# Kernel tuning notes

Measured on AMD Instinct MI355X. Metric: run time of the kernel, lower is better.

The kernel has to match this reference:

```python
import jax, jax.numpy as jnp
import numpy as np

B, L, E, R, A = 1024, 40, 1024, 1024, 512


def setup_inputs() -> dict:
    key = jax.random.key(0)
    ks = jax.random.split(key, 20)
    s = 0.05  # weight scale to avoid gate saturation
    inp = {
        "xt": jax.random.normal(ks[0], (B, E), jnp.float32),
        "xt_mask": jnp.ones((B, 1), jnp.float32),
        "V": jax.random.normal(ks[1], (B, L, R), jnp.float32),
        "pos_feat": jax.random.normal(ks[2], (B, R), jnp.float32),
        "h1": jax.random.normal(ks[3], (1, B, R), jnp.float32),
        "c1": jax.random.normal(ks[4], (1, B, R), jnp.float32),
        "h2": jax.random.normal(ks[5], (1, B, R), jnp.float32),
        "c2": jax.random.normal(ks[6], (1, B, R), jnp.float32),
        "Wg": jax.random.normal(ks[7], (E, R), jnp.float32) * s,
        "bg": jnp.zeros((R,), jnp.float32),
        "Wi1": jax.random.normal(ks[8], (E, 4 * R), jnp.float32) * s,
        "bi1": jnp.zeros((4 * R,), jnp.float32),
        "Wa1": jax.random.normal(ks[9], (R, 4 * R), jnp.float32) * s,
        "ba1": jnp.zeros((4 * R,), jnp.float32),
        "Wh1": jax.random.normal(ks[10], (R, 4 * R), jnp.float32) * s,
        "bh1": jnp.zeros((4 * R,), jnp.float32),
        "Wi2": jax.random.normal(ks[11], (R, 4 * R), jnp.float32) * s,
        "bi2": jnp.zeros((4 * R,), jnp.float32),
        "Wa2": jax.random.normal(ks[12], (R, 4 * R), jnp.float32) * s,
        "ba2": jnp.zeros((4 * R,), jnp.float32),
        "Wh2": jax.random.normal(ks[13], (R, 4 * R), jnp.float32) * s,
        "bh2": jnp.zeros((4 * R,), jnp.float32),
        "Wv2a": jax.random.normal(ks[14], (R, A), jnp.float32) * s,
        "bv2a": jnp.zeros((A,), jnp.float32),
        "Wh2a": jax.random.normal(ks[15], (2 * R, A), jnp.float32) * s,
        "bh2a": jnp.zeros((A,), jnp.float32),
        "Wa2w": jax.random.normal(ks[16], (A, 1), jnp.float32) * s,
        "ba2w": jnp.zeros((1,), jnp.float32),
    }
    return inp


def _lstm_cell(in1, in2, h, c, Wi, bi, Wa, ba, Wh, bh, mask):
    # all_input_sums: [B, 4R]; torch gate order: i, f, o (sigmoid) then g (tanh)
    s = in1 @ Wi + bi + in2 @ Wa + ba + h @ Wh + bh
    i_g = jax.nn.sigmoid(s[:, 0 * R:1 * R])
    f_g = jax.nn.sigmoid(s[:, 1 * R:2 * R])
    o_g = jax.nn.sigmoid(s[:, 2 * R:3 * R])
    g = jnp.tanh(s[:, 3 * R:4 * R])
    c_new = f_g * c + i_g * g
    c_new = c_new * mask + c * (1.0 - mask)
    h_new = o_g * jnp.tanh(c_new)
    h_new = h_new * mask + h * (1.0 - mask)
    return h_new, c_new


def reference(xt, xt_mask, V, pos_feat, h1, c1, h2, c2,
              Wg, bg, Wi1, bi1, Wa1, ba1, Wh1, bh1,
              Wi2, bi2, Wa2, ba2, Wh2, bh2,
              Wv2a, bv2a, Wh2a, bh2a, Wa2w, ba2w):
    h1l, c1l = h1[-1], c1[-1]  # [B, R]
    h2l, c2l = h2[-1], c2[-1]
    # additive attention over L frames
    hq = jnp.concatenate([h1l, h2l], axis=1) @ Wh2a + bh2a        # [B, A]
    e = jnp.tanh(hq[:, None, :] + V @ Wv2a + bv2a) @ Wa2w + ba2w  # [B, L, 1]
    w = jax.nn.softmax(e, axis=1)                                  # softmax over L
    af = jnp.sum(w * V, axis=1)                                    # [B, R]
    # gate (dropout in eval mode -> identity)
    gate = jax.nn.relu(xt @ Wg + bg)
    gated_pos = gate * pos_feat + pos_feat
    # two-layer LSTM
    out1, c1n = _lstm_cell(xt, gated_pos, h1l, c1l, Wi1, bi1, Wa1, ba1, Wh1, bh1, xt_mask)
    out2, c2n = _lstm_cell(out1, af, h2l, c2l, Wi2, bi2, Wa2, ba2, Wh2, bh2, xt_mask)
    return (out2, out1[None], c1n[None], out2[None], c2n[None])
```

## Files before the change

kernel.cpp:

```cpp
#include <hip/hip_runtime.h>
#include <math.h>

#define BB 1024
#define LL 40
#define RR 1024

using short8 = __attribute__((ext_vector_type(8))) short;
using us8    = __attribute__((ext_vector_type(8))) unsigned short;
using f32x4  = __attribute__((ext_vector_type(4))) float;

__device__ __forceinline__ ushort f2bf(float f) {
    union { float f; unsigned u; } a; a.f = f;
    unsigned r = a.u + 0x7fffu + ((a.u >> 16) & 1u);
    return (ushort)(r >> 16);
}
__device__ __forceinline__ float bf2f(ushort u) {
    union { unsigned u; float f; } a; a.u = ((unsigned)u) << 16;
    return a.f;
}
__device__ __forceinline__ float ftanh(float x) {
    float cx = fminf(fmaxf(x, -15.f), 15.f);
    float e = __expf(2.f * cx);
    return (e - 1.f) / (e + 1.f);
}
__device__ __forceinline__ float fsigmoid(float x) {
    float cx = fminf(fmaxf(x, -30.f), 30.f);
    return 1.f / (1.f + __expf(-cx));
}

__global__ __launch_bounds__(256) void conv_bf16_kernel(
    const float* __restrict__ src, ushort* __restrict__ dst, int n8)
{
    const int i = blockIdx.x * 256 + threadIdx.x;
    if (i >= n8) return;
    const float4* s4 = (const float4*)(src + (size_t)i * 8);
    float4 x = s4[0], y = s4[1];
    us8 v;
    v[0] = f2bf(x.x); v[1] = f2bf(x.y); v[2] = f2bf(x.z); v[3] = f2bf(x.w);
    v[4] = f2bf(y.x); v[5] = f2bf(y.y); v[6] = f2bf(y.z); v[7] = f2bf(y.w);
    ((us8*)dst)[i] = v;
}

struct CP3 { const float* in[3]; ushort* out[3]; };
__global__ __launch_bounds__(256) void conv_bf16_batch3_kernel(CP3 p, int n8)
{
    const int z = blockIdx.y;
    const int i = blockIdx.x * 256 + threadIdx.x;
    if (i >= n8) return;
    const float4* s4 = (const float4*)(p.in[z] + (size_t)i * 8);
    float4 x = s4[0], y = s4[1];
    us8 v;
    v[0] = f2bf(x.x); v[1] = f2bf(x.y); v[2] = f2bf(x.z); v[3] = f2bf(x.w);
    v[4] = f2bf(y.x); v[5] = f2bf(y.y); v[6] = f2bf(y.z); v[7] = f2bf(y.w);
    ((us8*)p.out[z])[i] = v;
}

struct TP6 { const float* in[6]; ushort* out[6]; int N[6]; };
__global__ __launch_bounds__(256) void transpose_conv_kernel(TP6 p)
{
    const int z = blockIdx.z;
    const int Nn = p.N[z];
    const int n0 = blockIdx.x * 64;
    if (n0 >= Nn) return;
    const int k0 = blockIdx.y * 64;
    const float* in = p.in[z];
    ushort* out = p.out[z];

    __shared__ float tile[64][65];
    const int t = threadIdx.x;
    const int tx = t & 63, ty = t >> 6;
#pragma unroll
    for (int r = 0; r < 16; ++r) {
        const int row = ty * 16 + r;
        tile[row][tx] = in[(size_t)(k0 + row) * Nn + n0 + tx];
    }
    __syncthreads();
    const int n = t >> 2, kq = t & 3;
    us8 v0, v1;
#pragma unroll
    for (int j = 0; j < 8; ++j) v0[j] = f2bf(tile[kq * 16 + j][n]);
#pragma unroll
    for (int j = 0; j < 8; ++j) v1[j] = f2bf(tile[kq * 16 + 8 + j][n]);
    ushort* op = out + (size_t)(n0 + n) * 1024 + k0 + kq * 16;
    *(us8*)op = v0;
    *((us8*)op + 1) = v1;
}

template <int NP, int EPI, int SK>
__global__ __launch_bounds__(256) void gemm_bf16(
    const ushort* __restrict__ A0, const ushort* __restrict__ A1, const ushort* __restrict__ A2,
    const ushort* __restrict__ W0, const ushort* __restrict__ W1, const ushort* __restrict__ W2,
    const float* __restrict__ b0, const float* __restrict__ b1, const float* __restrict__ b2,
    float* __restrict__ C, int M, int N,
    const float* __restrict__ hq, const float* __restrict__ bv2a,
    const float* __restrict__ Wa2w, float* __restrict__ epart)
{
    __shared__ ushort Alds[128 * 72];
    __shared__ ushort Blds[128 * 72];
    __shared__ float  red2[128][2];

    const int t = threadIdx.x;
    const int lane = t & 63;
    const int wave = t >> 6;
    const int wm = wave >> 1, wn = wave & 1;

    int bx, by;
    if constexpr (EPI == 2) {
        const int lin = blockIdx.y * 4 + blockIdx.x;
        const int nl = (lin & 7) * 160 + (lin >> 3);
        bx = nl & 3; by = nl >> 2;
    } else {
        bx = blockIdx.x; by = blockIdx.y;
    }
    const int m0 = by * 128, n0 = bx * 128;

    const int srow = t >> 1, skh = t & 1;
    const int soff = srow * 72 + skh * 32;

    f32x4 acc[4][4];
#pragma unroll
    for (int i = 0; i < 4; ++i)
#pragma unroll
        for (int j = 0; j < 4; ++j) acc[i][j] = (f32x4){0.f, 0.f, 0.f, 0.f};

    const int total = NP * 16;
    const int per   = total / SK;
    const int s0    = blockIdx.z * per;
    const int sEnd  = s0 + per;

    short8 ra[4], rw[4];
    {
        const int p  = (NP == 1) ? 0 : (s0 >> 4);
        const int k0 = (s0 & 15) << 6;
        const ushort* Ap = (p == 0) ? A0 : ((p == 1) ? A1 : A2);
        const ushort* Wp = (p == 0) ? W0 : ((p == 1) ? W1 : W2);
        const short8* ag = (const short8*)(Ap + (size_t)(m0 + srow) * 1024 + k0 + skh * 32);
        const short8* wg = (const short8*)(Wp + (size_t)(n0 + srow) * 1024 + k0 + skh * 32);
#pragma unroll
        for (int j = 0; j < 4; ++j) { ra[j] = ag[j]; rw[j] = wg[j]; }
    }

    for (int s = s0; s < sEnd; ++s) {
        __syncthreads();
#pragma unroll
        for (int j = 0; j < 4; ++j) {
            *(short8*)&Alds[soff + j * 8] = ra[j];
            *(short8*)&Blds[soff + j * 8] = rw[j];
        }
        __syncthreads();

        if (s + 1 < sEnd) {
            const int sn = s + 1;
            const int p  = (NP == 1) ? 0 : (sn >> 4);
            const int k0 = (sn & 15) << 6;
            const ushort* Ap = (p == 0) ? A0 : ((p == 1) ? A1 : A2);
            const ushort* Wp = (p == 0) ? W0 : ((p == 1) ? W1 : W2);
            const short8* ag = (const short8*)(Ap + (size_t)(m0 + srow) * 1024 + k0 + skh * 32);
            const short8* wg = (const short8*)(Wp + (size_t)(n0 + srow) * 1024 + k0 + skh * 32);
#pragma unroll
            for (int j = 0; j < 4; ++j) { ra[j] = ag[j]; rw[j] = wg[j]; }
        }

#pragma unroll
        for (int ks = 0; ks < 2; ++ks) {
            short8 aF[4], bF[4];
#pragma unroll
            for (int mi = 0; mi < 4; ++mi)
                aF[mi] = *(const short8*)&Alds[(wm * 64 + mi * 16 + (lane & 15)) * 72 + ks * 32 + (lane >> 4) * 8];
#pragma unroll
            for (int ni = 0; ni < 4; ++ni)
                bF[ni] = *(const short8*)&Blds[(wn * 64 + ni * 16 + (lane & 15)) * 72 + ks * 32 + (lane >> 4) * 8];
#pragma unroll
            for (int mi = 0; mi < 4; ++mi)
#pragma unroll
                for (int ni = 0; ni < 4; ++ni)
                    acc[mi][ni] = __builtin_amdgcn_mfma_f32_16x16x32_bf16(aF[mi], bF[ni], acc[mi][ni], 0, 0, 0);
        }
    }

    if constexpr (EPI == 0) {
#pragma unroll
        for (int ni = 0; ni < 4; ++ni) {
            const int col = n0 + wn * 64 + ni * 16 + (lane & 15);
            float bs = b0[col];
            if (NP > 1) bs += b1[col];
            if (NP > 2) bs += b2[col];
#pragma unroll
            for (int mi = 0; mi < 4; ++mi) {
                const int row = m0 + wm * 64 + mi * 16 + ((lane >> 4) << 2);
#pragma unroll
                for (int r = 0; r < 4; ++r)
                    C[(size_t)(row + r) * N + col] = acc[mi][ni][r] + bs;
            }
        }
    } else if constexpr (EPI == 3) {
        float* Cz = C + (size_t)blockIdx.z * M * N;
#pragma unroll
        for (int ni = 0; ni < 4; ++ni) {
            const int col = n0 + wn * 64 + ni * 16 + (lane & 15);
#pragma unroll
            for (int mi = 0; mi < 4; ++mi) {
                const int row = m0 + wm * 64 + mi * 16 + ((lane >> 4) << 2);
#pragma unroll
                for (int r = 0; r < 4; ++r)
                    Cz[(size_t)(row + r) * N + col] = acc[mi][ni][r];
            }
        }
    } else if constexpr (EPI == 2) {
        float wa[4], bv[4];
        int coln[4];
#pragma unroll
        for (int ni = 0; ni < 4; ++ni) {
            coln[ni] = n0 + wn * 64 + ni * 16 + (lane & 15);
            wa[ni] = Wa2w[coln[ni]];
            bv[ni] = bv2a[coln[ni]];
        }
#pragma unroll
        for (int mi = 0; mi < 4; ++mi) {
            const int rowb = m0 + wm * 64 + mi * 16 + ((lane >> 4) << 2);
#pragma unroll
            for (int r = 0; r < 4; ++r) {
                const int row = rowb + r;
                const int b = row / LL;
                float v = 0.f;
#pragma unroll
                for (int ni = 0; ni < 4; ++ni) {
                    float x = acc[mi][ni][r] + hq[(size_t)b * 512 + coln[ni]] + bv[ni];
                    v += ftanh(x) * wa[ni];
                }
                v += __shfl_xor(v, 1);
                v += __shfl_xor(v, 2);
                v += __shfl_xor(v, 4);
                v += __shfl_xor(v, 8);
                if ((lane & 15) == 0) red2[rowb - m0 + r][wn] = v;
            }
        }
        __syncthreads();
        if (t < 128)
            epart[(size_t)(m0 + t) * 4 + bx] = red2[t][0] + red2[t][1];
    }
}

__global__ __launch_bounds__(256) void reduce_hq_kernel(
    const float* __restrict__ part, const float* __restrict__ bias, float* __restrict__ hq)
{
    const int i = blockIdx.x * 256 + threadIdx.x;
    float s = bias[i & 511];
#pragma unroll
    for (int z = 0; z < 8; ++z) s += part[(size_t)z * 524288 + i];
    hq[i] = s;
}

__global__ __launch_bounds__(256) void reduce_gate_kernel(
    const float* __restrict__ part, const float* __restrict__ bias,
    const float* __restrict__ pos, ushort* __restrict__ gpb)
{
    const int i = blockIdx.x * 256 + threadIdx.x;
    float s = bias[i & 1023];
#pragma unroll
    for (int z = 0; z < 4; ++z) s += part[(size_t)z * 1048576 + i];
    const float g = fmaxf(s, 0.f);
    gpb[i] = f2bf(g * pos[i] + pos[i]);
}

__global__ __launch_bounds__(256) void softmax_af_kernel(
    const float* __restrict__ epart, const ushort* __restrict__ Vb,
    const float* __restrict__ ba2w, ushort* __restrict__ afb)
{
    const int b = blockIdx.x;
    const int tid = threadIdx.x;
    __shared__ float e_raw[LL];
    __shared__ float e_exp[LL];

    if (tid < LL) {
        const float* ep = &epart[(size_t)(b * LL + tid) * 4];
        float e = ba2w[0];
#pragma unroll
        for (int c = 0; c < 4; ++c) e += ep[c];
        e_raw[tid] = e;
    }
    __syncthreads();
    float mx = -1e30f;
#pragma unroll
    for (int l = 0; l < LL; ++l) mx = fmaxf(mx, e_raw[l]);
    if (tid < LL) e_exp[tid] = __expf(e_raw[tid] - mx);
    __syncthreads();
    float sum = 0.f;
#pragma unroll
    for (int l = 0; l < LL; ++l) sum += e_exp[l];
    const float inv = 1.f / sum;

    const int r4 = tid * 4;
    const ushort* vp = &Vb[(size_t)b * LL * RR + r4];
    float a0 = 0.f, a1 = 0.f, a2 = 0.f, a3 = 0.f;
#pragma unroll 8
    for (int l = 0; l < LL; ++l) {
        ushort4 v = *(const ushort4*)&vp[(size_t)l * RR];
        const float w = e_exp[l];
        a0 += w * bf2f(v.x); a1 += w * bf2f(v.y);
        a2 += w * bf2f(v.z); a3 += w * bf2f(v.w);
    }
    ushort* op = &afb[(size_t)b * RR + r4];
    op[0] = f2bf(a0 * inv); op[1] = f2bf(a1 * inv);
    op[2] = f2bf(a2 * inv); op[3] = f2bf(a3 * inv);
}

__global__ __launch_bounds__(256) void lstm_finish_kernel(
    const float* __restrict__ s, const float* __restrict__ c_in,
    const float* __restrict__ h_in, const float* __restrict__ mask,
    float* __restrict__ h_out, float* __restrict__ h_out2,
    float* __restrict__ c_out, ushort* __restrict__ h_bf)
{
    const int i = blockIdx.x * 256 + threadIdx.x;
    const int b = i >> 10;
    const int r = i & 1023;
    const float* sb = &s[(size_t)b * 4 * RR];
    const float ig = fsigmoid(sb[r]);
    const float fg = fsigmoid(sb[RR + r]);
    const float og = fsigmoid(sb[2 * RR + r]);
    const float g  = ftanh(sb[3 * RR + r]);
    const float m = mask[b];
    const float c = c_in[i];
    float cn = fg * c + ig * g;
    cn = cn * m + c * (1.f - m);
    const float h = h_in[i];
    float hn = og * ftanh(cn);
    hn = hn * m + h * (1.f - m);
    h_out[i] = hn;
    if (h_out2) h_out2[i] = hn;
    c_out[i] = cn;
    if (h_bf) h_bf[i] = f2bf(hn);
}

extern "C" void kernel_launch(void* const* d_in, const int* in_sizes, int n_in,
                              void* d_out, int out_size, void* d_ws, size_t ws_size,
                              hipStream_t stream) {
    const float* xt   = (const float*)d_in[0];
    const float* mask = (const float*)d_in[1];
    const float* V    = (const float*)d_in[2];
    const float* pos  = (const float*)d_in[3];
    const float* h1   = (const float*)d_in[4];
    const float* c1   = (const float*)d_in[5];
    const float* h2   = (const float*)d_in[6];
    const float* c2   = (const float*)d_in[7];
    const float* Wg   = (const float*)d_in[8];
    const float* bg   = (const float*)d_in[9];
    const float* Wi1  = (const float*)d_in[10];
    const float* bi1  = (const float*)d_in[11];
    const float* Wa1  = (const float*)d_in[12];
    const float* ba1  = (const float*)d_in[13];
    const float* Wh1  = (const float*)d_in[14];
    const float* bh1  = (const float*)d_in[15];
    const float* Wi2  = (const float*)d_in[16];
    const float* bi2  = (const float*)d_in[17];
    const float* Wa2  = (const float*)d_in[18];
    const float* ba2  = (const float*)d_in[19];
    const float* Wh2  = (const float*)d_in[20];
    const float* bh2  = (const float*)d_in[21];
    const float* Wv2a = (const float*)d_in[22];
    const float* bv2a = (const float*)d_in[23];
    const float* Wh2a = (const float*)d_in[24];
    const float* bh2a = (const float*)d_in[25];
    const float* Wa2w = (const float*)d_in[26];
    const float* ba2w = (const float*)d_in[27];

    float* out = (float*)d_out;
    float* out2  = out;
    float* out1  = out + (size_t)BB * RR;
    float* c1n   = out + 2 * (size_t)BB * RR;
    float* out2b = out + 3 * (size_t)BB * RR;
    float* c2n   = out + 4 * (size_t)BB * RR;

    ushort* wsu = (ushort*)d_ws;
    size_t o = 0;
    ushort* Vb     = wsu + o; o += (size_t)40960 * 1024;
    ushort* Wh2aT0 = wsu + o; o += (size_t)512 * 1024;
    ushort* Wh2aT1 = wsu + o; o += (size_t)512 * 1024;
    ushort* WgT    = wsu + o; o += (size_t)1024 * 1024;
    ushort* Wv2aT  = wsu + o; o += (size_t)512 * 1024;
    ushort* Wi1T   = wsu + o; o += (size_t)4096 * 1024;
    ushort* Wa1T   = wsu + o; o += (size_t)4096 * 1024;
    ushort* Wh1T   = wsu + o; o += (size_t)4096 * 1024;
    ushort* Wi2T   = wsu + o; o += (size_t)4096 * 1024;
    ushort* Wa2T   = wsu + o; o += (size_t)4096 * 1024;
    ushort* Wh2T   = wsu + o; o += (size_t)4096 * 1024;
    ushort* xtb    = wsu + o; o += (size_t)1024 * 1024;
    ushort* h1b    = wsu + o; o += (size_t)1024 * 1024;
    ushort* h2b    = wsu + o; o += (size_t)1024 * 1024;
    ushort* gpb    = wsu + o; o += (size_t)1024 * 1024;
    ushort* afb    = wsu + o; o += (size_t)1024 * 1024;
    ushort* out1b  = wsu + o; o += (size_t)1024 * 1024;
    float* wsf   = (float*)(wsu + o);
    float* hqf   = wsf;
    float* epart = hqf + 524288;
    float* sbuf  = epart + 163840;
    float* partK = sbuf;

    const dim3 blk(256);

    conv_bf16_kernel<<<dim3(20480), blk, 0, stream>>>(V, Vb, 5242880);
    {
        CP3 p; p.in[0] = xt; p.in[1] = h1; p.in[2] = h2;
        p.out[0] = xtb; p.out[1] = h1b; p.out[2] = h2b;
        conv_bf16_batch3_kernel<<<dim3(512, 3), blk, 0, stream>>>(p, 131072);
    }
    {
        TP6 p;
        p.in[0] = Wi1; p.in[1] = Wa1; p.in[2] = Wh1;
        p.in[3] = Wi2; p.in[4] = Wa2; p.in[5] = Wh2;
        p.out[0] = Wi1T; p.out[1] = Wa1T; p.out[2] = Wh1T;
        p.out[3] = Wi2T; p.out[4] = Wa2T; p.out[5] = Wh2T;
        for (int z = 0; z < 6; ++z) p.N[z] = 4096;
        transpose_conv_kernel<<<dim3(64, 16, 6), blk, 0, stream>>>(p);
    }
    {
        TP6 p;
        p.in[0] = Wh2a; p.in[1] = Wh2a + (size_t)1024 * 512;
        p.in[2] = Wg;   p.in[3] = Wv2a;
        p.out[0] = Wh2aT0; p.out[1] = Wh2aT1; p.out[2] = WgT; p.out[3] = Wv2aT;
        p.N[0] = 512; p.N[1] = 512; p.N[2] = 1024; p.N[3] = 512;
        p.in[4] = nullptr; p.in[5] = nullptr; p.out[4] = nullptr; p.out[5] = nullptr;
        p.N[4] = 0; p.N[5] = 0;
        transpose_conv_kernel<<<dim3(16, 16, 4), blk, 0, stream>>>(p);
    }

    gemm_bf16<2, 3, 8><<<dim3(4, 8, 8), blk, 0, stream>>>(
        h1b, h2b, nullptr, Wh2aT0, Wh2aT1, nullptr,
        nullptr, nullptr, nullptr, partK, 1024, 512, nullptr, nullptr, nullptr, nullptr);
    reduce_hq_kernel<<<dim3(2048), blk, 0, stream>>>(partK, bh2a, hqf);

    gemm_bf16<1, 3, 4><<<dim3(8, 8, 4), blk, 0, stream>>>(
        xtb, nullptr, nullptr, WgT, nullptr, nullptr,
        nullptr, nullptr, nullptr, partK, 1024, 1024, nullptr, nullptr, nullptr, nullptr);
    reduce_gate_kernel<<<dim3(4096), blk, 0, stream>>>(partK, bg, pos, gpb);

    gemm_bf16<1, 2, 1><<<dim3(4, 320, 1), blk, 0, stream>>>(
        Vb, nullptr, nullptr, Wv2aT, nullptr, nullptr,
        nullptr, nullptr, nullptr, nullptr, 40960, 512, hqf, bv2a, Wa2w, epart);
    softmax_af_kernel<<<dim3(BB), blk, 0, stream>>>(epart, Vb, ba2w, afb);

    gemm_bf16<3, 0, 1><<<dim3(32, 8, 1), blk, 0, stream>>>(
        xtb, gpb, h1b, Wi1T, Wa1T, Wh1T, bi1, ba1, bh1,
        sbuf, 1024, 4096, nullptr, nullptr, nullptr, nullptr);
    lstm_finish_kernel<<<dim3(4096), blk, 0, stream>>>(sbuf, c1, h1, mask, out1, nullptr, c1n, out1b);

    gemm_bf16<3, 0, 1><<<dim3(32, 8, 1), blk, 0, stream>>>(
        out1b, afb, h2b, Wi2T, Wa2T, Wh2T, bi2, ba2, bh2,
        sbuf, 1024, 4096, nullptr, nullptr, nullptr, nullptr);
    lstm_finish_kernel<<<dim3(4096), blk, 0, stream>>>(sbuf, c2, h2, mask, out2, out2b, c2n, nullptr);
}
```

Measured before the change: 323.2 us.

## Use direct global-to-LDS loads in GEMM and split-K the LSTM gate GEMMs

Rewrites the bf16 GEMM so operands go straight from global memory into LDS through global_load_lds, replacing the register-staged prefetch. K tiles shrink from 64 to 32 and the kernel no longer double-buffers. The two LSTM gate GEMMs now use 4-way split-K, which gives 1024 blocks instead of 256. Their partial sums land in the dead V bf16 buffer and are reduced, with the biases added, inside a new lstm_finish4 kernel. The gain is more parallelism and lower register pressure, paid for by extra partial-sum traffic and more barriers per K, with no load/compute overlap.

```diff
diff --git a/kernel.cpp b/kernel.cpp
--- a/kernel.cpp
+++ b/kernel.cpp
@@ -26,6 +26,13 @@
 __device__ __forceinline__ float fsigmoid(float x) {
     float cx = fminf(fmaxf(x, -30.f), 30.f);
     return 1.f / (1.f + __expf(-cx));
+}
+
+__device__ __forceinline__ void gll16(const ushort* g, ushort* l) {
+    __builtin_amdgcn_global_load_lds(
+        (const __attribute__((address_space(1))) void*)g,
+        (__attribute__((address_space(3))) void*)l,
+        16, 0, 0);
 }
 
 __global__ __launch_bounds__(256) void conv_bf16_kernel(
@@ -86,36 +93,30 @@
     *((us8*)op + 1) = v1;
 }
 
-template <int NP, int EPI, int SK>
-__global__ __launch_bounds__(256) void gemm_bf16(
+template <int NP, int SK, int EPI>
+__global__ __launch_bounds__(256) void gemm_gl(
     const ushort* __restrict__ A0, const ushort* __restrict__ A1, const ushort* __restrict__ A2,
     const ushort* __restrict__ W0, const ushort* __restrict__ W1, const ushort* __restrict__ W2,
-    const float* __restrict__ b0, const float* __restrict__ b1, const float* __restrict__ b2,
     float* __restrict__ C, int M, int N,
     const float* __restrict__ hq, const float* __restrict__ bv2a,
     const float* __restrict__ Wa2w, float* __restrict__ epart)
 {
-    __shared__ ushort Alds[128 * 72];
-    __shared__ ushort Blds[128 * 72];
-    __shared__ float  red2[128][2];
-
-    const int t = threadIdx.x;
-    const int lane = t & 63;
-    const int wave = t >> 6;
+    __shared__ ushort As[128 * 32];
+    __shared__ ushort Bs[128 * 32];
+
+    const int t = threadIdx.x, lane = t & 63, wave = t >> 6;
     const int wm = wave >> 1, wn = wave & 1;
 
     int bx, by;
     if constexpr (EPI == 2) {
-        const int lin = blockIdx.y * 4 + blockIdx.x;
-        const int nl = (lin & 7) * 160 + (lin >> 3);
-        bx = nl & 3; by = nl >> 2;
-    } else {
-        bx = blockIdx.x; by = blockIdx.y;
-    }
+        const int lin = blockIdx.y * gridDim.x + blockIdx.x;
+        const int swz = (lin & 7) * 160 + (lin >> 3);
+        bx = swz & 3; by = swz >> 2;
+    } else { bx = blockIdx.x; by = blockIdx.y; }
     const int m0 = by * 128, n0 = bx * 128;
 
-    const int srow = t >> 1, skh = t & 1;
-    const int soff = srow * 72 + skh * 32;
+    const int srow = 16 * wave + (lane >> 2);
+    const int skq  = lane & 3;
 
     f32x4 acc[4][4];
 #pragma unroll
@@ -123,77 +124,40 @@
 #pragma unroll
         for (int j = 0; j < 4; ++j) acc[i][j] = (f32x4){0.f, 0.f, 0.f, 0.f};
 
-    const int total = NP * 16;
+    const int total = NP * 32;
     const int per   = total / SK;
-    const int s0    = blockIdx.z * per;
-    const int sEnd  = s0 + per;
-
-    short8 ra[4], rw[4];
-    {
-        const int p  = (NP == 1) ? 0 : (s0 >> 4);
-        const int k0 = (s0 & 15) << 6;
+    const int s0v   = blockIdx.z * per;
+    const int sEnd  = s0v + per;
+
+    for (int s = s0v; s < sEnd; ++s) {
+        const int p  = (NP == 1) ? 0 : (s >> 5);
+        const int k0 = (s & 31) << 5;
         const ushort* Ap = (p == 0) ? A0 : ((p == 1) ? A1 : A2);
         const ushort* Wp = (p == 0) ? W0 : ((p == 1) ? W1 : W2);
-        const short8* ag = (const short8*)(Ap + (size_t)(m0 + srow) * 1024 + k0 + skh * 32);
-        const short8* wg = (const short8*)(Wp + (size_t)(n0 + srow) * 1024 + k0 + skh * 32);
-#pragma unroll
-        for (int j = 0; j < 4; ++j) { ra[j] = ag[j]; rw[j] = wg[j]; }
-    }
-
-    for (int s = s0; s < sEnd; ++s) {
+        const ushort* ga = Ap + (size_t)(m0 + srow) * 1024 + k0 + skq * 8;
+        const ushort* gb = Wp + (size_t)(n0 + srow) * 1024 + k0 + skq * 8;
+        gll16(ga,                 &As[512 * wave]);
+        gll16(ga + 64 * 1024,     &As[2048 + 512 * wave]);
+        gll16(gb,                 &Bs[512 * wave]);
+        gll16(gb + 64 * 1024,     &Bs[2048 + 512 * wave]);
         __syncthreads();
-#pragma unroll
-        for (int j = 0; j < 4; ++j) {
-            *(short8*)&Alds[soff + j * 8] = ra[j];
-            *(short8*)&Blds[soff + j * 8] = rw[j];
-        }
+
+        short8 aF[4], bF[4];
+#pragma unroll
+        for (int mi = 0; mi < 4; ++mi)
+            aF[mi] = *(const short8*)&As[(wm * 64 + mi * 16 + (lane & 15)) * 32 + (lane >> 4) * 8];
+#pragma unroll
+        for (int ni = 0; ni < 4; ++ni)
+            bF[ni] = *(const short8*)&Bs[(wn * 64 + ni * 16 + (lane & 15)) * 32 + (lane >> 4) * 8];
+#pragma unroll
+        for (int mi = 0; mi < 4; ++mi)
+#pragma unroll
+            for (int ni = 0; ni < 4; ++ni)
+                acc[mi][ni] = __builtin_amdgcn_mfma_f32_16x16x32_bf16(aF[mi], bF[ni], acc[mi][ni], 0, 0, 0);
         __syncthreads();
-
-        if (s + 1 < sEnd) {
-            const int sn = s + 1;
-            const int p  = (NP == 1) ? 0 : (sn >> 4);
-            const int k0 = (sn & 15) << 6;
-            const ushort* Ap = (p == 0) ? A0 : ((p == 1) ? A1 : A2);
-            const ushort* Wp = (p == 0) ? W0 : ((p == 1) ? W1 : W2);
-            const short8* ag = (const short8*)(Ap + (size_t)(m0 + srow) * 1024 + k0 + skh * 32);
-            const short8* wg = (const short8*)(Wp + (size_t)(n0 + srow) * 1024 + k0 + skh * 32);
-#pragma unroll
-            for (int j = 0; j < 4; ++j) { ra[j] = ag[j]; rw[j] = wg[j]; }
-        }
-
-#pragma unroll
-        for (int ks = 0; ks < 2; ++ks) {
-            short8 aF[4], bF[4];
-#pragma unroll
-            for (int mi = 0; mi < 4; ++mi)
-                aF[mi] = *(const short8*)&Alds[(wm * 64 + mi * 16 + (lane & 15)) * 72 + ks * 32 + (lane >> 4) * 8];
-#pragma unroll
-            for (int ni = 0; ni < 4; ++ni)
-                bF[ni] = *(const short8*)&Blds[(wn * 64 + ni * 16 + (lane & 15)) * 72 + ks * 32 + (lane >> 4) * 8];
-#pragma unroll
-            for (int mi = 0; mi < 4; ++mi)
-#pragma unroll
-                for (int ni = 0; ni < 4; ++ni)
-                    acc[mi][ni] = __builtin_amdgcn_mfma_f32_16x16x32_bf16(aF[mi], bF[ni], acc[mi][ni], 0, 0, 0);
-        }
-    }
-
-    if constexpr (EPI == 0) {
-#pragma unroll
-        for (int ni = 0; ni < 4; ++ni) {
-            const int col = n0 + wn * 64 + ni * 16 + (lane & 15);
-            float bs = b0[col];
-            if (NP > 1) bs += b1[col];
-            if (NP > 2) bs += b2[col];
-#pragma unroll
-            for (int mi = 0; mi < 4; ++mi) {
-                const int row = m0 + wm * 64 + mi * 16 + ((lane >> 4) << 2);
-#pragma unroll
-                for (int r = 0; r < 4; ++r)
-                    C[(size_t)(row + r) * N + col] = acc[mi][ni][r] + bs;
-            }
-        }
-    } else if constexpr (EPI == 3) {
+    }
+
+    if constexpr (EPI == 3) {
         float* Cz = C + (size_t)blockIdx.z * M * N;
 #pragma unroll
         for (int ni = 0; ni < 4; ++ni) {
@@ -207,6 +171,7 @@
             }
         }
     } else if constexpr (EPI == 2) {
+        float* red = (float*)As;
         float wa[4], bv[4];
         int coln[4];
 #pragma unroll
@@ -217,10 +182,10 @@
         }
 #pragma unroll
         for (int mi = 0; mi < 4; ++mi) {
-            const int rowb = m0 + wm * 64 + mi * 16 + ((lane >> 4) << 2);
+            const int rowl = wm * 64 + mi * 16 + ((lane >> 4) << 2);
 #pragma unroll
             for (int r = 0; r < 4; ++r) {
-                const int row = rowb + r;
+                const int row = m0 + rowl + r;
                 const int b = row / LL;
                 float v = 0.f;
 #pragma unroll
@@ -232,12 +197,12 @@
                 v += __shfl_xor(v, 2);
                 v += __shfl_xor(v, 4);
                 v += __shfl_xor(v, 8);
-                if ((lane & 15) == 0) red2[rowb - m0 + r][wn] = v;
+                if ((lane & 15) == 0) red[(rowl + r) * 2 + wn] = v;
             }
         }
         __syncthreads();
         if (t < 128)
-            epart[(size_t)(m0 + t) * 4 + bx] = red2[t][0] + red2[t][1];
+            epart[(size_t)(m0 + t) * 4 + bx] = red[t * 2] + red[t * 2 + 1];
     }
 }
 
@@ -305,23 +270,33 @@
     op[2] = f2bf(a2 * inv); op[3] = f2bf(a3 * inv);
 }
 
-__global__ __launch_bounds__(256) void lstm_finish_kernel(
-    const float* __restrict__ s, const float* __restrict__ c_in,
-    const float* __restrict__ h_in, const float* __restrict__ mask,
+__global__ __launch_bounds__(256) void lstm_finish4_kernel(
+    const float* __restrict__ part,
+    const float* __restrict__ bi, const float* __restrict__ ba, const float* __restrict__ bh,
+    const float* __restrict__ c_in, const float* __restrict__ h_in, const float* __restrict__ mask,
     float* __restrict__ h_out, float* __restrict__ h_out2,
     float* __restrict__ c_out, ushort* __restrict__ h_bf)
 {
     const int i = blockIdx.x * 256 + threadIdx.x;
     const int b = i >> 10;
     const int r = i & 1023;
-    const float* sb = &s[(size_t)b * 4 * RR];
-    const float ig = fsigmoid(sb[r]);
-    const float fg = fsigmoid(sb[RR + r]);
-    const float og = fsigmoid(sb[2 * RR + r]);
-    const float g  = ftanh(sb[3 * RR + r]);
+    float sg[4];
+#pragma unroll
+    for (int g = 0; g < 4; ++g) {
+        const int gr = g * 1024 + r;
+        float s = bi[gr] + ba[gr] + bh[gr];
+#pragma unroll
+        for (int z = 0; z < 4; ++z)
+            s += part[(size_t)z * 4194304 + (size_t)b * 4096 + gr];
+        sg[g] = s;
+    }
+    const float ig = fsigmoid(sg[0]);
+    const float fg = fsigmoid(sg[1]);
+    const float og = fsigmoid(sg[2]);
+    const float gt = ftanh(sg[3]);
     const float m = mask[b];
     const float c = c_in[i];
-    float cn = fg * c + ig * g;
+    float cn = fg * c + ig * gt;
     cn = cn * m + c * (1.f - m);
     const float h = h_in[i];
     float hn = og * ftanh(cn);
@@ -390,11 +365,11 @@
     ushort* gpb    = wsu + o; o += (size_t)1024 * 1024;
     ushort* afb    = wsu + o; o += (size_t)1024 * 1024;
     ushort* out1b  = wsu + o; o += (size_t)1024 * 1024;
-    float* wsf   = (float*)(wsu + o);
-    float* hqf   = wsf;
-    float* epart = hqf + 524288;
-    float* sbuf  = epart + 163840;
-    float* partK = sbuf;
+    float* wsf    = (float*)(wsu + o);
+    float* hqf    = wsf;
+    float* epart  = hqf + 524288;
+    float* partSm = epart + 163840;
+    float* partK  = (float*)Vb;
 
     const dim3 blk(256);
 
@@ -424,28 +399,30 @@
         transpose_conv_kernel<<<dim3(16, 16, 4), blk, 0, stream>>>(p);
     }
 
-    gemm_bf16<2, 3, 8><<<dim3(4, 8, 8), blk, 0, stream>>>(
+    gemm_gl<2, 8, 3><<<dim3(4, 8, 8), blk, 0, stream>>>(
         h1b, h2b, nullptr, Wh2aT0, Wh2aT1, nullptr,
-        nullptr, nullptr, nullptr, partK, 1024, 512, nullptr, nullptr, nullptr, nullptr);
-    reduce_hq_kernel<<<dim3(2048), blk, 0, stream>>>(partK, bh2a, hqf);
-
-    gemm_bf16<1, 3, 4><<<dim3(8, 8, 4), blk, 0, stream>>>(
+        partSm, 1024, 512, nullptr, nullptr, nullptr, nullptr);
+    reduce_hq_kernel<<<dim3(2048), blk, 0, stream>>>(partSm, bh2a, hqf);
+
+    gemm_gl<1, 4, 3><<<dim3(8, 8, 4), blk, 0, stream>>>(
         xtb, nullptr, nullptr, WgT, nullptr, nullptr,
-        nullptr, nullptr, nullptr, partK, 1024, 1024, nullptr, nullptr, nullptr, nullptr);
-    reduce_gate_kernel<<<dim3(4096), blk, 0, stream>>>(partK, bg, pos, gpb);
-
-    gemm_bf16<1, 2, 1><<<dim3(4, 320, 1), blk, 0, stream>>>(
+        partSm, 1024, 1024, nullptr, nullptr, nullptr, nullptr);
+    reduce_gate_kernel<<<dim3(4096), blk, 0, stream>>>(partSm, bg, pos, gpb);
+
+    gemm_gl<1, 1, 2><<<dim3(4, 320, 1), blk, 0, stream>>>(
         Vb, nullptr, nullptr, Wv2aT, nullptr, nullptr,
-        nullptr, nullptr, nullptr, nullptr, 40960, 512, hqf, bv2a, Wa2w, epart);
+        nullptr, 40960, 512, hqf, bv2a, Wa2w, epart);
     softmax_af_kernel<<<dim3(BB), blk, 0, stream>>>(epart, Vb, ba2w, afb);
 
-    gemm_bf16<3, 0, 1><<<dim3(32, 8, 1), blk, 0, stream>>>(
-        xtb, gpb, h1b, Wi1T, Wa1T, Wh1T, bi1, ba1, bh1,
-        sbuf, 1024, 4096, nullptr, nullptr, nullptr, nullptr);
-    lstm_finish_kernel<<<dim3(4096), blk, 0, stream>>>(sbuf, c1, h1, mask, out1, nullptr, c1n, out1b);
-
-    gemm_bf16<3, 0, 1><<<dim3(32, 8, 1), blk, 0, stream>>>(
-        out1b, afb, h2b, Wi2T, Wa2T, Wh2T, bi2, ba2, bh2,
-        sbuf, 1024, 4096, nullptr, nullptr, nullptr, nullptr);
-    lstm_finish_kernel<<<dim3(4096), blk, 0, stream>>>(sbuf, c2, h2, mask, out2, out2b, c2n, nullptr);
-}
+    gemm_gl<3, 4, 3><<<dim3(32, 8, 4), blk, 0, stream>>>(
+        xtb, gpb, h1b, Wi1T, Wa1T, Wh1T,
+        partK, 1024, 4096, nullptr, nullptr, nullptr, nullptr);
+    lstm_finish4_kernel<<<dim3(4096), blk, 0, stream>>>(
+        partK, bi1, ba1, bh1, c1, h1, mask, out1, nullptr, c1n, out1b);
+
+    gemm_gl<3, 4, 3><<<dim3(32, 8, 4), blk, 0, stream>>>(
+        out1b, afb, h2b, Wi2T, Wa2T, Wh2T,
+        partK, 1024, 4096, nullptr, nullptr, nullptr, nullptr);
+    lstm_finish4_kernel<<<dim3(4096), blk, 0, stream>>>(
+        partK, bi2, ba2, bh2, c2, h2, mask, out2, out2b, c2n, nullptr);
+}
```

New measurement: 329.0 us. Within noise of the previous version (+1.8%).
